# Kernel tuning notes

Hardware: AMD Instinct MI355X
Metric: run time of the kernel (lower is better)

The kernel has to match this reference:

```python
import jax, jax.numpy as jnp
import numpy as np

N_NODES = 50000
N_EDGES = 800000
HIDDEN = 128
N_GRAPHS = 128


def setup_inputs() -> dict:
    key = jax.random.key(0)
    ks = jax.random.split(key, 12)
    x = jax.random.normal(ks[0], (N_NODES, HIDDEN), dtype=jnp.float32)
    edge_index = jax.random.randint(ks[1], (2, N_EDGES), 0, N_NODES, dtype=jnp.int64)
    batch = jnp.sort(jax.random.randint(ks[2], (N_NODES,), 0, N_GRAPHS, dtype=jnp.int64))
    s = 1.0 / np.sqrt(HIDDEN)
    def lin(k):
        return jax.random.uniform(k, (HIDDEN, HIDDEN), jnp.float32, -s, s)
    return {
        "x": x,
        "edge_index": edge_index,
        "batch": batch,
        # layer 1 SAGEConv: lin_l (neighbor, with bias), lin_r (root, no bias)
        "wl1": lin(ks[3]), "b1": jax.random.uniform(ks[4], (HIDDEN,), jnp.float32, -s, s), "wr1": lin(ks[5]),
        # layer 2 SAGEConv
        "wl2": lin(ks[6]), "b2": jax.random.uniform(ks[7], (HIDDEN,), jnp.float32, -s, s), "wr2": lin(ks[8]),
        # classifier Linear
        "cw": lin(ks[9]), "cb": jax.random.uniform(ks[10], (HIDDEN,), jnp.float32, -s, s),
    }


def _sage_conv(x, src, dst, wl, b, wr, n_nodes):
    # mean aggregation of source features onto destination nodes
    agg = jax.ops.segment_sum(x[src], dst, num_segments=n_nodes)      # [N, H]
    deg = jax.ops.segment_sum(jnp.ones_like(dst, x.dtype), dst, num_segments=n_nodes)
    mean = agg / jnp.maximum(deg, 1.0)[:, None]
    # out = lin_l(mean) + lin_r(x); lin_l carries the bias (PyG convention)
    return mean @ wl.T + b + x @ wr.T


def reference(x, edge_index, batch, wl1, b1, wr1, wl2, b2, wr2, cw, cb):
    src, dst = edge_index[0], edge_index[1]
    n = x.shape[0]
    h = jax.nn.relu(_sage_conv(x, src, dst, wl1, b1, wr1, n))
    h = jax.nn.relu(_sage_conv(h, src, dst, wl2, b2, wr2, n))
    # global mean pool over graphs (dropout p=0.0 -> identity)
    gsum = jax.ops.segment_sum(h, batch, num_segments=N_GRAPHS)       # [G, H]
    gcnt = jax.ops.segment_sum(jnp.ones((n,), h.dtype), batch, num_segments=N_GRAPHS)
    pooled = gsum / jnp.maximum(gcnt, 1.0)[:, None]
    return pooled @ cw.T + cb
```

## Files before the change

kernel.cpp:

```cpp
#include <hip/hip_runtime.h>
#include <cstdint>
#include <cstddef>

#define HID 128
#define LDK 72
#define EPB 4096
#define CAP 8192

typedef __attribute__((ext_vector_type(8))) short short8;
typedef __attribute__((ext_vector_type(4))) float floatx4;

#if __has_builtin(__builtin_amdgcn_cvt_pk_f32_fp8) && __has_builtin(__builtin_amdgcn_cvt_pk_fp8_f32)
#define HW_FP8 1
#else
#define HW_FP8 0
#endif

__device__ __forceinline__ unsigned short f2bf(float f) {
  union { float f; uint32_t u; } c; c.f = f;
  uint32_t u = c.u;
  uint32_t r = (u + 0x7FFFu + ((u >> 16) & 1u)) >> 16;
  return (unsigned short)r;
}
__device__ __forceinline__ float bflo(uint32_t v) { return __uint_as_float(v << 16); }
__device__ __forceinline__ float bfhi(uint32_t v) { return __uint_as_float(v & 0xFFFF0000u); }
__device__ __forceinline__ float bf2f(unsigned short s) { return __uint_as_float(((uint32_t)s) << 16); }

__device__ __forceinline__ uint32_t f2fp8_sw(float v) {
  uint32_t u = __float_as_uint(v);
  uint32_t s = (u >> 24) & 0x80u;
  uint32_t af = u & 0x7FFFFFFFu;
  if (__uint_as_float(af) < 0.015625f) return s;
  uint32_t r = af + 0x7FFFFu + ((af >> 20) & 1u);
  return s | ((r >> 20) - 960u);
}
__device__ __forceinline__ float fp8dec_sw(uint32_t b) {
  uint32_t mag = b & 0x7Fu;
  uint32_t v = ((b & 0x80u) << 24) | ((mag << 20) + 0x3C000000u);
  return mag ? __uint_as_float(v) : 0.0f;
}

__device__ __forceinline__ uint32_t pack_fp8x4(float a, float b, float c, float d) {
#if HW_FP8
  int p = __builtin_amdgcn_cvt_pk_fp8_f32(a, b, 0, false);
  p = __builtin_amdgcn_cvt_pk_fp8_f32(c, d, p, true);
  return (uint32_t)p;
#else
  return f2fp8_sw(a) | (f2fp8_sw(b) << 8) | (f2fp8_sw(c) << 16) | (f2fp8_sw(d) << 24);
#endif
}

__device__ __forceinline__ unsigned char f2fp8_one(float v) {
#if HW_FP8
  return (unsigned char)(__builtin_amdgcn_cvt_pk_fp8_f32(v, v, 0, false) & 0xFF);
#else
  return (unsigned char)f2fp8_sw(v);
#endif
}

__device__ __forceinline__ void acc_fp8x4(float* __restrict__ a, uint32_t w) {
#if HW_FP8
  auto lo = __builtin_amdgcn_cvt_pk_f32_fp8(w, false);
  auto hi = __builtin_amdgcn_cvt_pk_f32_fp8(w, true);
  a[0] += lo[0]; a[1] += lo[1]; a[2] += hi[0]; a[3] += hi[1];
#else
  a[0] += fp8dec_sw(w & 255);
  a[1] += fp8dec_sw((w >> 8) & 255);
  a[2] += fp8dec_sw((w >> 16) & 255);
  a[3] += fp8dec_sw(w >> 24);
#endif
}


__global__ __launch_bounds__(256) void k_bucket(const int* __restrict__ src,
                                                const int* __restrict__ dst,
                                                int* __restrict__ bcur,
                                                uint32_t* __restrict__ ebuf,
                                                int E, int NB) {
  __shared__ int hist[256];
  __shared__ int lcur[256];
  const int t = threadIdx.x;
  const int base = blockIdx.x * EPB;
  hist[t] = 0;
  __syncthreads();

  uint32_t val[EPB / 256];
  int bk[EPB / 256];
  #pragma unroll
  for (int i = 0; i < EPB / 256; ++i) {
    int e = base + i * 256 + t;
    bk[i] = -1;
    if (e < E) {
      int d = dst[e];
      int s = src[e];
      bk[i] = d >> 8;
      val[i] = (uint32_t)s | ((uint32_t)(d & 255) << 16);
      atomicAdd(&hist[bk[i]], 1);
    }
  }
  __syncthreads();
  if (t < NB) {
    int c = hist[t];
    lcur[t] = c ? atomicAdd(&bcur[t], c) : 0;
  }
  __syncthreads();
  #pragma unroll
  for (int i = 0; i < EPB / 256; ++i) {
    if (bk[i] >= 0) {
      int pos = bk[i] * CAP + atomicAdd(&lcur[bk[i]], 1);
      ebuf[pos] = val[i];
    }
  }
}

__global__ __launch_bounds__(256) void k_bucket_fill2(const uint32_t* __restrict__ ebuf,
                                                      const int* __restrict__ bcur,
                                                      int* __restrict__ rowbeg,
                                                      int* __restrict__ rowend,
                                                      unsigned short* __restrict__ csr16,
                                                      int N) {
  __shared__ int hist[256];
  __shared__ int scan[256];
  const int b = blockIdx.x;
  const int t = threadIdx.x;
  hist[t] = 0;
  __syncthreads();
  const int lo = b * CAP;
  const int hi = lo + bcur[b];
  for (int i = lo + t; i < hi; i += 256) atomicAdd(&hist[ebuf[i] >> 16], 1);
  __syncthreads();
  int v = hist[t];
  scan[t] = v;
  __syncthreads();
  #pragma unroll
  for (int off = 1; off < 256; off <<= 1) {
    int add = (t >= off) ? scan[t - off] : 0;
    __syncthreads();
    scan[t] += add;
    __syncthreads();
  }
  int excl = scan[t] - v;
  int node = (b << 8) + t;
  if (node < N) {
    rowbeg[node] = lo + excl;
    rowend[node] = lo + excl + v;
  }
  hist[t] = lo + excl;
  __syncthreads();
  for (int i = lo + t; i < hi; i += 256) {
    uint32_t e = ebuf[i];
    int pos = atomicAdd(&hist[e >> 16], 1);
    csr16[pos] = (unsigned short)(e & 0xFFFFu);
  }
}


__global__ __launch_bounds__(256) void k_cast_dual(const float* __restrict__ src,
                                                   unsigned short* __restrict__ dst,
                                                   uint32_t* __restrict__ q, int n4) {
  int i = blockIdx.x * 256 + threadIdx.x;
  if (i < n4) {
    float4 v = ((const float4*)src)[i];
    uint32_t lo = (uint32_t)f2bf(v.x) | ((uint32_t)f2bf(v.y) << 16);
    uint32_t hi = (uint32_t)f2bf(v.z) | ((uint32_t)f2bf(v.w) << 16);
    ((uint2*)dst)[i] = make_uint2(lo, hi);
    q[i] = pack_fp8x4(v.x, v.y, v.z, v.w);
  }
}


__global__ __launch_bounds__(256) void k_aggregate(const unsigned char* __restrict__ featq,
                                                   const int* __restrict__ rowbeg,
                                                   const int* __restrict__ rowend,
                                                   const unsigned short* __restrict__ csr16,
                                                   unsigned short* __restrict__ outmean, int N) {
  int wpair = blockIdx.x * 4 + (threadIdx.x >> 6);
  int n0 = wpair * 2;
  int n1 = n0 + 1;
  int lane = threadIdx.x & 63;
  if (n0 >= N) return;
  const int grp = lane >> 4;
  const int fl  = lane & 15;

  int b0 = rowbeg[n0], e0 = rowend[n0];
  int b1 = 0, e1 = 0;
  if (n1 < N) { b1 = rowbeg[n1]; e1 = rowend[n1]; }
  const int d0 = e0 - b0, d1 = e1 - b1;

  float a0[8], a1[8];
  #pragma unroll
  for (int i = 0; i < 8; ++i) { a0[i] = 0.f; a1[i] = 0.f; }

  while (b0 < e0 || b1 < e1) {
    int m0 = e0 - b0; if (m0 < 0) m0 = 0; if (m0 > 64) m0 = 64;
    int m1 = e1 - b1; if (m1 < 0) m1 = 0; if (m1 > 64) m1 = 64;
    int sidx0 = (b0 + lane < e0) ? (int)csr16[b0 + lane] : 0;
    int sidx1 = (b1 + lane < e1) ? (int)csr16[b1 + lane] : 0;
    int mm = m0 > m1 ? m0 : m1;
    for (int j = 0; j < mm; j += 16) {
      int j0 = j + grp, j1 = j + grp + 4, j2 = j + grp + 8, j3 = j + grp + 12;
      int s00 = __shfl(sidx0, j0, 64), s01 = __shfl(sidx0, j1, 64);
      int s02 = __shfl(sidx0, j2, 64), s03 = __shfl(sidx0, j3, 64);
      int s10 = __shfl(sidx1, j0, 64), s11 = __shfl(sidx1, j1, 64);
      int s12 = __shfl(sidx1, j2, 64), s13 = __shfl(sidx1, j3, 64);
      bool p00 = j0 < m0, p01 = j1 < m0, p02 = j2 < m0, p03 = j3 < m0;
      bool p10 = j0 < m1, p11 = j1 < m1, p12 = j2 < m1, p13 = j3 < m1;
      uint2 u00, u01, u02, u03, u10, u11, u12, u13;
      if (p00) u00 = *(const uint2*)(featq + (size_t)s00 * HID + fl * 8);
      if (p01) u01 = *(const uint2*)(featq + (size_t)s01 * HID + fl * 8);
      if (p02) u02 = *(const uint2*)(featq + (size_t)s02 * HID + fl * 8);
      if (p03) u03 = *(const uint2*)(featq + (size_t)s03 * HID + fl * 8);
      if (p10) u10 = *(const uint2*)(featq + (size_t)s10 * HID + fl * 8);
      if (p11) u11 = *(const uint2*)(featq + (size_t)s11 * HID + fl * 8);
      if (p12) u12 = *(const uint2*)(featq + (size_t)s12 * HID + fl * 8);
      if (p13) u13 = *(const uint2*)(featq + (size_t)s13 * HID + fl * 8);
      if (p00) { acc_fp8x4(a0, u00.x); acc_fp8x4(a0 + 4, u00.y); }
      if (p01) { acc_fp8x4(a0, u01.x); acc_fp8x4(a0 + 4, u01.y); }
      if (p02) { acc_fp8x4(a0, u02.x); acc_fp8x4(a0 + 4, u02.y); }
      if (p03) { acc_fp8x4(a0, u03.x); acc_fp8x4(a0 + 4, u03.y); }
      if (p10) { acc_fp8x4(a1, u10.x); acc_fp8x4(a1 + 4, u10.y); }
      if (p11) { acc_fp8x4(a1, u11.x); acc_fp8x4(a1 + 4, u11.y); }
      if (p12) { acc_fp8x4(a1, u12.x); acc_fp8x4(a1 + 4, u12.y); }
      if (p13) { acc_fp8x4(a1, u13.x); acc_fp8x4(a1 + 4, u13.y); }
    }
    b0 += 64; b1 += 64;
  }

  #pragma unroll
  for (int i = 0; i < 8; ++i) {
    a0[i] += __shfl_xor(a0[i], 16, 64);
    a0[i] += __shfl_xor(a0[i], 32, 64);
    a1[i] += __shfl_xor(a1[i], 16, 64);
    a1[i] += __shfl_xor(a1[i], 32, 64);
  }
  if (grp == 0) {
    float inv0 = 1.0f / (float)(d0 > 1 ? d0 : 1);
    uint4 o;
    o.x = (uint32_t)f2bf(a0[0] * inv0) | ((uint32_t)f2bf(a0[1] * inv0) << 16);
    o.y = (uint32_t)f2bf(a0[2] * inv0) | ((uint32_t)f2bf(a0[3] * inv0) << 16);
    o.z = (uint32_t)f2bf(a0[4] * inv0) | ((uint32_t)f2bf(a0[5] * inv0) << 16);
    o.w = (uint32_t)f2bf(a0[6] * inv0) | ((uint32_t)f2bf(a0[7] * inv0) << 16);
    *(uint4*)(outmean + (size_t)n0 * HID + fl * 8) = o;
    if (n1 < N) {
      float inv1 = 1.0f / (float)(d1 > 1 ? d1 : 1);
      uint4 p;
      p.x = (uint32_t)f2bf(a1[0] * inv1) | ((uint32_t)f2bf(a1[1] * inv1) << 16);
      p.y = (uint32_t)f2bf(a1[2] * inv1) | ((uint32_t)f2bf(a1[3] * inv1) << 16);
      p.z = (uint32_t)f2bf(a1[4] * inv1) | ((uint32_t)f2bf(a1[5] * inv1) << 16);
      p.w = (uint32_t)f2bf(a1[6] * inv1) | ((uint32_t)f2bf(a1[7] * inv1) << 16);
      *(uint4*)(outmean + (size_t)n1 * HID + fl * 8) = p;
    }
  }
}


__global__ __launch_bounds__(256, 2) void k_gemm_mfma(const unsigned short* __restrict__ A1,
                                                      const unsigned short* __restrict__ A2,
                                                      const float* __restrict__ WL,
                                                      const float* __restrict__ WR,
                                                      const float* __restrict__ bias,
                                                      unsigned short* __restrict__ outb,
                                                      unsigned char* __restrict__ outq,
                                                      const int* __restrict__ batch,
                                                      float* __restrict__ pooled,
                                                      int M, int relu) {
  __shared__ __align__(16) unsigned short sAB[2 * 128 * LDK];
  __shared__ int sB[128];
  unsigned short* sA = sAB;
  unsigned short* sW = sAB + 128 * LDK;
  const int t = threadIdx.x;
  const int lane = t & 63;
  const int wave = t >> 6;
  const int row0 = blockIdx.x * 128;
  const int mhalf = (wave & 1) * 64;
  const int nhalf = (wave >> 1) * 64;
  const int ml = lane & 15;
  const int q  = lane >> 4;

  floatx4 acc[4][4];
  #pragma unroll
  for (int a = 0; a < 4; ++a)
    #pragma unroll
    for (int b = 0; b < 4; ++b) acc[a][b] = (floatx4){0.f, 0.f, 0.f, 0.f};

  for (int stage = 0; stage < 4; ++stage) {
    const unsigned short* __restrict__ Asrc = (stage < 2) ? A1 : A2;
    const float* __restrict__ Wsrc = (stage < 2) ? WL : WR;
    const int k0g = (stage & 1) * 64;
    if (stage) __syncthreads();

    #pragma unroll
    for (int i = 0; i < 4; ++i) {
      int seg = t + i * 256;
      int r = seg >> 3, kc = (seg & 7) * 8;
      int gr = row0 + r;
      float4 v = make_float4(0.f, 0.f, 0.f, 0.f);
      if (gr < M) v = *(const float4*)(Asrc + (size_t)gr * HID + k0g + kc);
      *(float4*)&sA[r * LDK + kc] = v;
    }
    #pragma unroll
    for (int i = 0; i < 8; ++i) {
      int e = t + i * 256;
      int o = e >> 4, kc = (e & 15) * 4;
      float4 v = *(const float4*)(Wsrc + (size_t)o * HID + k0g + kc);
      uint32_t lo = (uint32_t)f2bf(v.x) | ((uint32_t)f2bf(v.y) << 16);
      uint32_t hi = (uint32_t)f2bf(v.z) | ((uint32_t)f2bf(v.w) << 16);
      *(uint2*)&sW[o * LDK + kc] = make_uint2(lo, hi);
    }
    __syncthreads();

    #pragma unroll
    for (int ks = 0; ks < 2; ++ks) {
      int kb = ks * 32 + q * 8;
      short8 af[4], bfr[4];
      #pragma unroll
      for (int mt = 0; mt < 4; ++mt)
        af[mt] = *(const short8*)&sA[(mhalf + mt * 16 + ml) * LDK + kb];
      #pragma unroll
      for (int nt = 0; nt < 4; ++nt)
        bfr[nt] = *(const short8*)&sW[(nhalf + nt * 16 + ml) * LDK + kb];
      #pragma unroll
      for (int mt = 0; mt < 4; ++mt)
        #pragma unroll
        for (int nt = 0; nt < 4; ++nt)
          acc[mt][nt] = __builtin_amdgcn_mfma_f32_16x16x32_bf16(af[mt], bfr[nt], acc[mt][nt], 0, 0, 0);
    }
  }

  if (pooled == nullptr) {
    #pragma unroll
    for (int nt = 0; nt < 4; ++nt) {
      int gcol = nhalf + nt * 16 + ml;
      float bv = bias[gcol];
      #pragma unroll
      for (int mt = 0; mt < 4; ++mt) {
        #pragma unroll
        for (int r = 0; r < 4; ++r) {
          int grow = row0 + mhalf + mt * 16 + q * 4 + r;
          if (grow < M) {
            float v = acc[mt][nt][r] + bv;
            if (relu) v = fmaxf(v, 0.f);
            outb[(size_t)grow * HID + gcol] = f2bf(v);
            if (outq) outq[(size_t)grow * HID + gcol] = f2fp8_one(v);
          }
        }
      }
    }
  } else {
    __syncthreads();
    unsigned short* sH = sAB;
    #pragma unroll
    for (int nt = 0; nt < 4; ++nt) {
      int gcol = nhalf + nt * 16 + ml;
      float bv = bias[gcol];
      #pragma unroll
      for (int mt = 0; mt < 4; ++mt) {
        #pragma unroll
        for (int r = 0; r < 4; ++r) {
          int lr = mhalf + mt * 16 + q * 4 + r;
          float v = acc[mt][nt][r] + bv;
          if (relu) v = fmaxf(v, 0.f);
          sH[lr * 128 + gcol] = f2bf(v);
        }
      }
    }
    if (t < 128) sB[t] = (row0 + t < M) ? batch[row0 + t] : -1;
    __syncthreads();
    const int f = t & 127, half = t >> 7;
    float pacc = 0.f;
    int curg = -1;
    for (int n = half; n < 128; n += 2) {
      int g = sB[n];
      if (g != curg) {
        if (curg >= 0) atomicAdd(&pooled[(size_t)curg * HID + f], pacc);
        curg = g; pacc = 0.f;
      }
      if (g >= 0) pacc += bf2f(sH[n * 128 + f]);
    }
    if (curg >= 0) atomicAdd(&pooled[(size_t)curg * HID + f], pacc);
  }
}


__device__ __forceinline__ int lower_bound_dev(const int* a, int n, int key) {
  int lo = 0, hi = n;
  while (lo < hi) {
    int mid = (lo + hi) >> 1;
    if (a[mid] < key) lo = mid + 1; else hi = mid;
  }
  return lo;
}

__global__ __launch_bounds__(256) void k_classify(const float* __restrict__ pooled,
                                                  const int* __restrict__ batch,
                                                  const float* __restrict__ cw,
                                                  const float* __restrict__ cb,
                                                  float* __restrict__ out, int N) {
  __shared__ int bnds[2];
  __shared__ float sp[128];
  __shared__ float part[2][128];
  int g = blockIdx.x;
  int t = threadIdx.x;
  if (t == 0) bnds[0] = lower_bound_dev(batch, N, g);
  if (t == 1) bnds[1] = lower_bound_dev(batch, N, g + 1);
  __syncthreads();
  int cnt = bnds[1] - bnds[0];
  float inv = 1.0f / (float)(cnt > 1 ? cnt : 1);
  if (t < 128) sp[t] = pooled[(size_t)g * HID + t] * inv;
  __syncthreads();
  int o = t & 127, kh = t >> 7;
  float a = 0.f;
  #pragma unroll 4
  for (int k = kh * 64; k < kh * 64 + 64; ++k) a += sp[k] * cw[(size_t)o * HID + k];
  part[kh][o] = a;
  __syncthreads();
  if (t < 128) out[(size_t)g * HID + t] = part[0][t] + part[1][t] + cb[t];
}


extern "C" void kernel_launch(void* const* d_in, const int* in_sizes, int n_in,
                              void* d_out, int out_size, void* d_ws, size_t ws_size,
                              hipStream_t stream) {
  const float* x     = (const float*)d_in[0];
  const int*   ei    = (const int*)d_in[1];
  const int*   batch = (const int*)d_in[2];
  const float* wl1   = (const float*)d_in[3];
  const float* b1    = (const float*)d_in[4];
  const float* wr1   = (const float*)d_in[5];
  const float* wl2   = (const float*)d_in[6];
  const float* b2    = (const float*)d_in[7];
  const float* wr2   = (const float*)d_in[8];
  const float* cw    = (const float*)d_in[9];
  const float* cb    = (const float*)d_in[10];
  float* out = (float*)d_out;

  const int N = in_sizes[0] / HID;
  const int E = in_sizes[1] / 2;
  const int G = out_size / HID;
  const int* src = ei;
  const int* dst = ei + E;

  char* w = (char*)d_ws;
  int*      bcur   = (int*)(w);
  float*    pooled = (float*)(w + 1024);
  int*      rowbeg = (int*)(w + 66560);
  int*      rowend = (int*)(w + 266560);
  uint32_t* ebuf   = (uint32_t*)(w + 466944);
  unsigned short* csr16 = (unsigned short*)(w + 6889472);
  unsigned short* xb    = (unsigned short*)(w + 10100736);
  unsigned short* meanb = (unsigned short*)(w + 10100736 + 12800000);
  unsigned short* h1b   = (unsigned short*)(w + 10100736 + 25600000);
  unsigned char*  xq    = (unsigned char*)(w + 10100736 + 38400000);
  unsigned char*  h1q   = (unsigned char*)(w + 10100736 + 44800000);

  const int NB = (N + 255) >> 8;
  const int nPairs = (N + 1) / 2;
  const int aggBlocks  = (nPairs + 3) / 4;
  const int gemmBlocks = (N + 127) / 128;
  const int castBlocks = (N * HID / 4 + 255) / 256;
  const int bktBlocks  = (E + EPB - 1) / EPB;

  hipMemsetAsync(w, 0, 66560, stream);

  hipLaunchKernelGGL(k_bucket,       dim3(bktBlocks), dim3(256), 0, stream, src, dst, bcur, ebuf, E, NB);
  hipLaunchKernelGGL(k_bucket_fill2, dim3(NB),  dim3(256), 0, stream, ebuf, bcur, rowbeg, rowend, csr16, N);
  hipLaunchKernelGGL(k_cast_dual,    dim3(castBlocks), dim3(256), 0, stream, x, xb, (uint32_t*)xq, N * HID / 4);

  hipLaunchKernelGGL(k_aggregate, dim3(aggBlocks), dim3(256), 0, stream, xq, rowbeg, rowend, csr16, meanb, N);
  hipLaunchKernelGGL(k_gemm_mfma, dim3(gemmBlocks), dim3(256), 0, stream, meanb, xb, wl1, wr1, b1, h1b, h1q,
                     (const int*)nullptr, (float*)nullptr, N, 1);
  hipLaunchKernelGGL(k_aggregate, dim3(aggBlocks), dim3(256), 0, stream, h1q, rowbeg, rowend, csr16, meanb, N);
  hipLaunchKernelGGL(k_gemm_mfma, dim3(gemmBlocks), dim3(256), 0, stream, meanb, h1b, wl2, wr2, b2,
                     (unsigned short*)nullptr, (unsigned char*)nullptr, batch, pooled, N, 1);
  hipLaunchKernelGGL(k_classify, dim3(G), dim3(256), 0, stream, pooled, batch, cw, cb, out, N);
}
```

Measured before the change: 227.0 us.

## Store all intermediate activations as fp8 and fuse cast into bucket kernel

Drops the bf16 copies of x, mean and h1. The GEMM now loads fp8 activations and expands them to bf16 in shared memory. The aggregation writes its mean output as fp8 instead of bf16. The separate cast kernel is merged into the bucketing launch as extra blocks, which removes one launch and the bf16 write of x. This roughly halves activation memory traffic, at the cost of lower precision on the root term and the mean inputs to the GEMMs.

```diff
diff --git a/kernel.cpp b/kernel.cpp
--- a/kernel.cpp
+++ b/kernel.cpp
@@ -22,9 +22,10 @@
   uint32_t r = (u + 0x7FFFu + ((u >> 16) & 1u)) >> 16;
   return (unsigned short)r;
 }
-__device__ __forceinline__ float bflo(uint32_t v) { return __uint_as_float(v << 16); }
-__device__ __forceinline__ float bfhi(uint32_t v) { return __uint_as_float(v & 0xFFFF0000u); }
 __device__ __forceinline__ float bf2f(unsigned short s) { return __uint_as_float(((uint32_t)s) << 16); }
+__device__ __forceinline__ uint32_t pkbf(float a, float b) {
+  return (__float_as_uint(a) >> 16) | (__float_as_uint(b) & 0xFFFF0000u);
+}
 
 __device__ __forceinline__ uint32_t f2fp8_sw(float v) {
   uint32_t u = __float_as_uint(v);
@@ -71,15 +72,48 @@
 #endif
 }
 
-
-__global__ __launch_bounds__(256) void k_bucket(const int* __restrict__ src,
-                                                const int* __restrict__ dst,
-                                                int* __restrict__ bcur,
-                                                uint32_t* __restrict__ ebuf,
-                                                int E, int NB) {
+__device__ __forceinline__ uint4 fp8x8_to_bf16x8(uint2 w) {
+#if HW_FP8
+  auto f01 = __builtin_amdgcn_cvt_pk_f32_fp8(w.x, false);
+  auto f23 = __builtin_amdgcn_cvt_pk_f32_fp8(w.x, true);
+  auto f45 = __builtin_amdgcn_cvt_pk_f32_fp8(w.y, false);
+  auto f67 = __builtin_amdgcn_cvt_pk_f32_fp8(w.y, true);
+  uint4 o;
+  o.x = pkbf(f01[0], f01[1]);
+  o.y = pkbf(f23[0], f23[1]);
+  o.z = pkbf(f45[0], f45[1]);
+  o.w = pkbf(f67[0], f67[1]);
+  return o;
+#else
+  uint4 o;
+  o.x = pkbf(fp8dec_sw(w.x & 255), fp8dec_sw((w.x >> 8) & 255));
+  o.y = pkbf(fp8dec_sw((w.x >> 16) & 255), fp8dec_sw(w.x >> 24));
+  o.z = pkbf(fp8dec_sw(w.y & 255), fp8dec_sw((w.y >> 8) & 255));
+  o.w = pkbf(fp8dec_sw((w.y >> 16) & 255), fp8dec_sw(w.y >> 24));
+  return o;
+#endif
+}
+
+
+__global__ __launch_bounds__(256) void k_bucket_cast(const int* __restrict__ src,
+                                                     const int* __restrict__ dst,
+                                                     int* __restrict__ bcur,
+                                                     uint32_t* __restrict__ ebuf,
+                                                     int E, int NB,
+                                                     const float* __restrict__ x,
+                                                     uint32_t* __restrict__ xq,
+                                                     int n4, int bktBlocks) {
+  const int t = threadIdx.x;
+  if ((int)blockIdx.x >= bktBlocks) {
+    int i = ((int)blockIdx.x - bktBlocks) * 256 + t;
+    if (i < n4) {
+      float4 v = ((const float4*)x)[i];
+      xq[i] = pack_fp8x4(v.x, v.y, v.z, v.w);
+    }
+    return;
+  }
   __shared__ int hist[256];
   __shared__ int lcur[256];
-  const int t = threadIdx.x;
   const int base = blockIdx.x * EPB;
   hist[t] = 0;
   __syncthreads();
@@ -155,25 +189,11 @@
 }
 
 
-__global__ __launch_bounds__(256) void k_cast_dual(const float* __restrict__ src,
-                                                   unsigned short* __restrict__ dst,
-                                                   uint32_t* __restrict__ q, int n4) {
-  int i = blockIdx.x * 256 + threadIdx.x;
-  if (i < n4) {
-    float4 v = ((const float4*)src)[i];
-    uint32_t lo = (uint32_t)f2bf(v.x) | ((uint32_t)f2bf(v.y) << 16);
-    uint32_t hi = (uint32_t)f2bf(v.z) | ((uint32_t)f2bf(v.w) << 16);
-    ((uint2*)dst)[i] = make_uint2(lo, hi);
-    q[i] = pack_fp8x4(v.x, v.y, v.z, v.w);
-  }
-}
-
-
 __global__ __launch_bounds__(256) void k_aggregate(const unsigned char* __restrict__ featq,
                                                    const int* __restrict__ rowbeg,
                                                    const int* __restrict__ rowend,
                                                    const unsigned short* __restrict__ csr16,
-                                                   unsigned short* __restrict__ outmean, int N) {
+                                                   unsigned char* __restrict__ outmean, int N) {
   int wpair = blockIdx.x * 4 + (threadIdx.x >> 6);
   int n0 = wpair * 2;
   int n1 = n0 + 1;
@@ -235,31 +255,26 @@
   }
   if (grp == 0) {
     float inv0 = 1.0f / (float)(d0 > 1 ? d0 : 1);
-    uint4 o;
-    o.x = (uint32_t)f2bf(a0[0] * inv0) | ((uint32_t)f2bf(a0[1] * inv0) << 16);
-    o.y = (uint32_t)f2bf(a0[2] * inv0) | ((uint32_t)f2bf(a0[3] * inv0) << 16);
-    o.z = (uint32_t)f2bf(a0[4] * inv0) | ((uint32_t)f2bf(a0[5] * inv0) << 16);
-    o.w = (uint32_t)f2bf(a0[6] * inv0) | ((uint32_t)f2bf(a0[7] * inv0) << 16);
-    *(uint4*)(outmean + (size_t)n0 * HID + fl * 8) = o;
+    uint2 o;
+    o.x = pack_fp8x4(a0[0] * inv0, a0[1] * inv0, a0[2] * inv0, a0[3] * inv0);
+    o.y = pack_fp8x4(a0[4] * inv0, a0[5] * inv0, a0[6] * inv0, a0[7] * inv0);
+    *(uint2*)(outmean + (size_t)n0 * HID + fl * 8) = o;
     if (n1 < N) {
       float inv1 = 1.0f / (float)(d1 > 1 ? d1 : 1);
-      uint4 p;
-      p.x = (uint32_t)f2bf(a1[0] * inv1) | ((uint32_t)f2bf(a1[1] * inv1) << 16);
-      p.y = (uint32_t)f2bf(a1[2] * inv1) | ((uint32_t)f2bf(a1[3] * inv1) << 16);
-      p.z = (uint32_t)f2bf(a1[4] * inv1) | ((uint32_t)f2bf(a1[5] * inv1) << 16);
-      p.w = (uint32_t)f2bf(a1[6] * inv1) | ((uint32_t)f2bf(a1[7] * inv1) << 16);
-      *(uint4*)(outmean + (size_t)n1 * HID + fl * 8) = p;
-    }
-  }
-}
-
-
-__global__ __launch_bounds__(256, 2) void k_gemm_mfma(const unsigned short* __restrict__ A1,
-                                                      const unsigned short* __restrict__ A2,
+      uint2 p;
+      p.x = pack_fp8x4(a1[0] * inv1, a1[1] * inv1, a1[2] * inv1, a1[3] * inv1);
+      p.y = pack_fp8x4(a1[4] * inv1, a1[5] * inv1, a1[6] * inv1, a1[7] * inv1);
+      *(uint2*)(outmean + (size_t)n1 * HID + fl * 8) = p;
+    }
+  }
+}
+
+
+__global__ __launch_bounds__(256, 2) void k_gemm_mfma(const unsigned char* __restrict__ A1q,
+                                                      const unsigned char* __restrict__ A2q,
                                                       const float* __restrict__ WL,
                                                       const float* __restrict__ WR,
                                                       const float* __restrict__ bias,
-                                                      unsigned short* __restrict__ outb,
                                                       unsigned char* __restrict__ outq,
                                                       const int* __restrict__ batch,
                                                       float* __restrict__ pooled,
@@ -284,7 +299,7 @@
     for (int b = 0; b < 4; ++b) acc[a][b] = (floatx4){0.f, 0.f, 0.f, 0.f};
 
   for (int stage = 0; stage < 4; ++stage) {
-    const unsigned short* __restrict__ Asrc = (stage < 2) ? A1 : A2;
+    const unsigned char* __restrict__ Aq = (stage < 2) ? A1q : A2q;
     const float* __restrict__ Wsrc = (stage < 2) ? WL : WR;
     const int k0g = (stage & 1) * 64;
     if (stage) __syncthreads();
@@ -294,9 +309,9 @@
       int seg = t + i * 256;
       int r = seg >> 3, kc = (seg & 7) * 8;
       int gr = row0 + r;
-      float4 v = make_float4(0.f, 0.f, 0.f, 0.f);
-      if (gr < M) v = *(const float4*)(Asrc + (size_t)gr * HID + k0g + kc);
-      *(float4*)&sA[r * LDK + kc] = v;
+      uint2 wv = make_uint2(0u, 0u);
+      if (gr < M) wv = *(const uint2*)(Aq + (size_t)gr * HID + k0g + kc);
+      *(uint4*)&sA[r * LDK + kc] = fp8x8_to_bf16x8(wv);
     }
     #pragma unroll
     for (int i = 0; i < 8; ++i) {
@@ -340,8 +355,7 @@
           if (grow < M) {
             float v = acc[mt][nt][r] + bv;
             if (relu) v = fmaxf(v, 0.f);
-            outb[(size_t)grow * HID + gcol] = f2bf(v);
-            if (outq) outq[(size_t)grow * HID + gcol] = f2fp8_one(v);
+            outq[(size_t)grow * HID + gcol] = f2fp8_one(v);
           }
         }
       }
@@ -447,11 +461,9 @@
   int*      rowend = (int*)(w + 266560);
   uint32_t* ebuf   = (uint32_t*)(w + 466944);
   unsigned short* csr16 = (unsigned short*)(w + 6889472);
-  unsigned short* xb    = (unsigned short*)(w + 10100736);
-  unsigned short* meanb = (unsigned short*)(w + 10100736 + 12800000);
-  unsigned short* h1b   = (unsigned short*)(w + 10100736 + 25600000);
-  unsigned char*  xq    = (unsigned char*)(w + 10100736 + 38400000);
-  unsigned char*  h1q   = (unsigned char*)(w + 10100736 + 44800000);
+  unsigned char* xq    = (unsigned char*)(w + 10100736);
+  unsigned char* meanq = (unsigned char*)(w + 10100736 + 6400000);
+  unsigned char* h1q   = (unsigned char*)(w + 10100736 + 12800000);
 
   const int NB = (N + 255) >> 8;
   const int nPairs = (N + 1) / 2;
@@ -462,15 +474,15 @@
 
   hipMemsetAsync(w, 0, 66560, stream);
 
-  hipLaunchKernelGGL(k_bucket,       dim3(bktBlocks), dim3(256), 0, stream, src, dst, bcur, ebuf, E, NB);
-  hipLaunchKernelGGL(k_bucket_fill2, dim3(NB),  dim3(256), 0, stream, ebuf, bcur, rowbeg, rowend, csr16, N);
-  hipLaunchKernelGGL(k_cast_dual,    dim3(castBlocks), dim3(256), 0, stream, x, xb, (uint32_t*)xq, N * HID / 4);
-
-  hipLaunchKernelGGL(k_aggregate, dim3(aggBlocks), dim3(256), 0, stream, xq, rowbeg, rowend, csr16, meanb, N);
-  hipLaunchKernelGGL(k_gemm_mfma, dim3(gemmBlocks), dim3(256), 0, stream, meanb, xb, wl1, wr1, b1, h1b, h1q,
+  hipLaunchKernelGGL(k_bucket_cast, dim3(bktBlocks + castBlocks), dim3(256), 0, stream,
+                     src, dst, bcur, ebuf, E, NB, x, (uint32_t*)xq, N * HID / 4, bktBlocks);
+  hipLaunchKernelGGL(k_bucket_fill2, dim3(NB), dim3(256), 0, stream, ebuf, bcur, rowbeg, rowend, csr16, N);
+
+  hipLaunchKernelGGL(k_aggregate, dim3(aggBlocks), dim3(256), 0, stream, xq, rowbeg, rowend, csr16, meanq, N);
+  hipLaunchKernelGGL(k_gemm_mfma, dim3(gemmBlocks), dim3(256), 0, stream, meanq, xq, wl1, wr1, b1, h1q,
                      (const int*)nullptr, (float*)nullptr, N, 1);
-  hipLaunchKernelGGL(k_aggregate, dim3(aggBlocks), dim3(256), 0, stream, h1q, rowbeg, rowend, csr16, meanb, N);
-  hipLaunchKernelGGL(k_gemm_mfma, dim3(gemmBlocks), dim3(256), 0, stream, meanb, h1b, wl2, wr2, b2,
-                     (unsigned short*)nullptr, (unsigned char*)nullptr, batch, pooled, N, 1);
+  hipLaunchKernelGGL(k_aggregate, dim3(aggBlocks), dim3(256), 0, stream, h1q, rowbeg, rowend, csr16, meanq, N);
+  hipLaunchKernelGGL(k_gemm_mfma, dim3(gemmBlocks), dim3(256), 0, stream, meanq, h1q, wl2, wr2, b2,
+                     (unsigned char*)nullptr, batch, pooled, N, 1);
   hipLaunchKernelGGL(k_classify, dim3(G), dim3(256), 0, stream, pooled, batch, cw, cb, out, N);
 }
```

Measured after the change: 215.2 us. 5.2% less time.
